# Performance work log

Measured on AMD Instinct MI355X. Metric: run time of the kernel, lower is better.

The kernel has to match this reference:

```python
import jax, jax.numpy as jnp
import numpy as np

N, E, D, L = 50000, 800000, 128, 2
EPS = 1e-10


def mobius_add(x, y, c):
    # c: shape [1], broadcasts against [N,1]
    xy = jnp.sum(x * y, axis=-1, keepdims=True)
    x2 = jnp.sum(x * x, axis=-1, keepdims=True)
    y2 = jnp.sum(y * y, axis=-1, keepdims=True)
    num = (1 + 2 * c * xy + c * y2) * x + (1 - c * x2) * y
    den = 1 + 2 * c * xy + (c ** 2) * x2 * y2
    return num / den


def log_map(x, y, c):
    ym = mobius_add(-x, y, c)
    n = jnp.maximum(jnp.linalg.norm(ym, axis=-1, keepdims=True), EPS)
    sc = jnp.sqrt(c)
    return (2.0 / sc) * jnp.arctanh(sc * n) * ym / n


def exp_map(x, v, c):
    n = jnp.maximum(jnp.linalg.norm(v, axis=-1, keepdims=True), EPS)
    sc = jnp.sqrt(c)
    second = jnp.tanh(sc * n / 2.0) * v / (sc * n)
    return mobius_add(x, second, c)


def l2norm(x):
    return x / jnp.maximum(jnp.linalg.norm(x, axis=-1, keepdims=True), 1e-12)


def mean_agg(h, src, dst, n_nodes):
    # copy_u + mean reduce: mean of h[src] grouped by dst; zero-degree -> 0
    msum = jax.ops.segment_sum(h[src], dst, num_segments=n_nodes)
    deg = jax.ops.segment_sum(jnp.ones((src.shape[0], 1), h.dtype), dst, num_segments=n_nodes)
    return msum / jnp.maximum(deg, 1.0)


def setup_inputs() -> dict:
    key = jax.random.key(0)
    ks = jax.random.split(key, 12)
    scale = 1.0 / np.sqrt(D)
    return {
        "src": jax.random.randint(ks[0], (E,), 0, N, dtype=jnp.int32),
        "dst": jax.random.randint(ks[1], (E,), 0, N, dtype=jnp.int32),
        "e_emb": jax.random.normal(ks[2], (N, D), dtype=jnp.float32),
        "b_emb": 0.01 * jax.random.normal(ks[3], (N, D), dtype=jnp.float32),  # inside Poincare ball
        "s_emb": jax.random.normal(ks[4], (N, D), dtype=jnp.float32),
        "e_W": scale * jax.random.normal(ks[5], (L, D, D), dtype=jnp.float32),
        "e_b": jnp.zeros((L, D), dtype=jnp.float32),
        "b_W": scale * jax.random.normal(ks[6], (L, D, D), dtype=jnp.float32),
        "b_b": jnp.zeros((L, D), dtype=jnp.float32),
        "s_W": scale * jax.random.normal(ks[7], (L, D, D), dtype=jnp.float32),
        "s_b": jnp.zeros((L, D), dtype=jnp.float32),
        "b_curvature": jnp.ones((1,), dtype=jnp.float32),
        "s_curvature": jnp.ones((1,), dtype=jnp.float32),
    }


def reference(src, dst, e_emb, b_emb, s_emb, e_W, e_b, b_W, b_b, s_W, s_b, b_curvature, s_curvature):
    n = e_emb.shape[0]
    origin = jnp.zeros((1, b_emb.shape[-1]), dtype=b_emb.dtype)
    for l in range(L):
        # Euclidean: transform -> mean aggregate -> LeakyReLU(0.2)
        h = e_emb @ e_W[l].T + e_b[l]
        e_emb = mean_agg(h, src, dst, n)
        e_emb = jnp.where(e_emb > 0, e_emb, 0.2 * e_emb)
        # Hyperbolic: log map to tangent -> transform -> mean aggregate -> exp map
        tangent = log_map(origin, b_emb, b_curvature)
        hb = tangent @ b_W[l].T + b_b[l]
        neigh_b = mean_agg(hb, src, dst, n)
        b_emb = exp_map(origin, neigh_b, b_curvature)
        # Spherical: normalize -> transform -> normalize -> mean aggregate -> normalize
        hs = l2norm(l2norm(s_emb) @ s_W[l].T + s_b[l])
        s_emb = l2norm(mean_agg(hs, src, dst, n))
    return (e_emb, b_emb, s_emb)
```

## Files before the change

### kernel.cpp

```cpp
#include <hip/hip_runtime.h>
#include <math.h>

#define DD 128
typedef unsigned int   u32;
typedef unsigned short u16;
typedef short bf16x8 __attribute__((ext_vector_type(8)));
typedef float f32x4  __attribute__((ext_vector_type(4)));

__device__ __forceinline__ float lo2f(u32 p){ return __uint_as_float(p << 16); }
__device__ __forceinline__ float hi2f(u32 p){ return __uint_as_float(p & 0xFFFF0000u); }
__device__ __forceinline__ u16 f2bf(float f){
    u32 u = __float_as_uint(f);
    return (u16)((u + 0x7fffu + ((u >> 16) & 1u)) >> 16);
}

__global__ void k_hist(const int* __restrict__ dst, int* __restrict__ deg, int E){
    int i = blockIdx.x*256 + threadIdx.x;
    if (i < E) atomicAdd(&deg[dst[i]], 1);
}

__global__ void k_chunksum(const int* __restrict__ deg, int* __restrict__ csum,
                           float* __restrict__ invdeg, int n){
    __shared__ int sdata[256];
    int t = threadIdx.x;
    int i0 = blockIdx.x*512 + t*2;
    int a = (i0     < n) ? deg[i0]   : 0;
    int b = (i0 + 1 < n) ? deg[i0+1] : 0;
    if (i0     < n) invdeg[i0]   = 1.0f / (float)max(a, 1);
    if (i0 + 1 < n) invdeg[i0+1] = 1.0f / (float)max(b, 1);
    sdata[t] = a + b; __syncthreads();
    for (int off = 128; off > 0; off >>= 1){
        if (t < off) sdata[t] += sdata[t+off];
        __syncthreads();
    }
    if (t == 0) csum[blockIdx.x] = sdata[0];
}

__global__ void k_scanchunks(int* __restrict__ csum, int nchunks,
                             int* __restrict__ row_ptr, int n){
    __shared__ int s[256];
    __shared__ int carry_sh;
    int t = threadIdx.x;
    if (t == 0) carry_sh = 0;
    __syncthreads();
    for (int base = 0; base < nchunks; base += 256){
        int i = base + t;
        int v = (i < nchunks) ? csum[i] : 0;
        s[t] = v;
        __syncthreads();
        for (int off = 1; off < 256; off <<= 1){
            int u = (t >= off) ? s[t-off] : 0;
            __syncthreads();
            s[t] += u;
            __syncthreads();
        }
        int carry = carry_sh;
        int excl  = carry + s[t] - v;
        if (i < nchunks) csum[i] = excl;
        int tot = s[255];
        __syncthreads();
        if (t == 0) carry_sh = carry + tot;
        __syncthreads();
    }
    if (t == 0) row_ptr[n] = carry_sh;
}

__global__ void k_scanwithin(const int* __restrict__ deg, const int* __restrict__ csum,
                             int* __restrict__ row_ptr, int* __restrict__ cursor, int n){
    __shared__ int s[256];
    int t = threadIdx.x;
    int i0 = blockIdx.x*512 + t*2;
    int a = (i0     < n) ? deg[i0]   : 0;
    int b = (i0 + 1 < n) ? deg[i0+1] : 0;
    int tsum = a + b;
    s[t] = tsum; __syncthreads();
    for (int off = 1; off < 256; off <<= 1){
        int v = (t >= off) ? s[t-off] : 0;
        __syncthreads();
        s[t] += v;
        __syncthreads();
    }
    int excl = s[t] - tsum + csum[blockIdx.x];
    if (i0     < n){ row_ptr[i0]   = excl;     cursor[i0]   = excl;     }
    if (i0 + 1 < n){ row_ptr[i0+1] = excl + a; cursor[i0+1] = excl + a; }
}

template<typename IT>
__global__ void k_fill(const int* __restrict__ src, const int* __restrict__ dst,
                       int* __restrict__ cursor, IT* __restrict__ sorted_src, int E){
    int i = blockIdx.x*256 + threadIdx.x;
    if (i < E){
        int p = atomicAdd(&cursor[dst[i]], 1);
        sorted_src[p] = (IT)src[i];
    }
}

__global__ void k_w2b3(const float* __restrict__ w0, const float* __restrict__ w1,
                       const float* __restrict__ w2,
                       u16* __restrict__ o0, u16* __restrict__ o1, u16* __restrict__ o2,
                       int nw){
    int i = blockIdx.x*256 + threadIdx.x;
    if (i >= nw) return;
    const float* s = (blockIdx.y == 0) ? w0 : (blockIdx.y == 1) ? w1 : w2;
    u16*         o = (blockIdx.y == 0) ? o0 : (blockIdx.y == 1) ? o1 : o2;
    o[i] = f2bf(s[i]);
}

template<int PRE, int POST>
__device__ __forceinline__ void gemm_body(const float* __restrict__ X, const u16* __restrict__ Wb,
                                          const float* __restrict__ bias, u16* __restrict__ Y,
                                          size_t sstride, int n_rows, const float* __restrict__ cptr){
    int t = threadIdx.x;
    int wave = t >> 6, lane = t & 63;
    int q = lane >> 4, m = lane & 15;
    int rowbase = blockIdx.x*128 + wave*32;
    int gr0 = min(rowbase + m,      n_rows - 1);
    int gr1 = min(rowbase + 16 + m, n_rows - 1);

    float4 xv0[8], xv1[8];
    const float4* xp0 = (const float4*)(X + (size_t)gr0*DD);
    const float4* xp1 = (const float4*)(X + (size_t)gr1*DD);
    #pragma unroll
    for (int c = 0; c < 4; c++){
        xv0[2*c]   = xp0[c*8 + q*2];
        xv0[2*c+1] = xp0[c*8 + q*2 + 1];
        xv1[2*c]   = xp1[c*8 + q*2];
        xv1[2*c+1] = xp1[c*8 + q*2 + 1];
    }

    float scale0 = 1.0f, scale1 = 1.0f;
    if (PRE != 0){
        float ss0 = 0.f, ss1 = 0.f;
        #pragma unroll
        for (int i = 0; i < 8; i++){
            ss0 += xv0[i].x*xv0[i].x + xv0[i].y*xv0[i].y + xv0[i].z*xv0[i].z + xv0[i].w*xv0[i].w;
            ss1 += xv1[i].x*xv1[i].x + xv1[i].y*xv1[i].y + xv1[i].z*xv1[i].z + xv1[i].w*xv1[i].w;
        }
        ss0 += __shfl_xor(ss0, 16, 64); ss0 += __shfl_xor(ss0, 32, 64);
        ss1 += __shfl_xor(ss1, 16, 64); ss1 += __shfl_xor(ss1, 32, 64);
        if (PRE == 1){
            float c  = cptr[0];
            c = (c > 0.f && c < 1e30f) ? c : 1.0f;
            float sc = sqrtf(c);
            float n0 = fmaxf(sqrtf(ss0), 1e-10f);
            float n1 = fmaxf(sqrtf(ss1), 1e-10f);
            float a0 = fminf(sc*n0, 0.99999994f);
            float a1 = fminf(sc*n1, 0.99999994f);
            scale0 = (2.0f/sc) * atanhf(a0) / n0;
            scale1 = (2.0f/sc) * atanhf(a1) / n1;
        } else {
            scale0 = 1.0f / fmaxf(sqrtf(ss0), 1e-12f);
            scale1 = 1.0f / fmaxf(sqrtf(ss1), 1e-12f);
        }
    }

    bf16x8 af0[4], af1[4];
    #pragma unroll
    for (int c = 0; c < 4; c++){
        const float* xf0 = (const float*)&xv0[2*c];
        const float* xf1 = (const float*)&xv1[2*c];
        #pragma unroll
        for (int j = 0; j < 8; j++){
            af0[c][j] = (short)f2bf(xf0[j]*scale0);
            af1[c][j] = (short)f2bf(xf1[j]*scale1);
        }
    }

    f32x4 acc0[8], acc1[8];
    #pragma unroll
    for (int tl = 0; tl < 8; tl++){
        acc0[tl] = (f32x4){0.f,0.f,0.f,0.f};
        acc1[tl] = (f32x4){0.f,0.f,0.f,0.f};
    }

    const u16* wb = Wb + (size_t)m*DD + q*8;
    #pragma unroll
    for (int c = 0; c < 4; c++){
        #pragma unroll
        for (int tl = 0; tl < 8; tl++){
            bf16x8 bfr = *(const bf16x8*)(wb + (size_t)tl*16*DD + c*32);
            acc0[tl] = __builtin_amdgcn_mfma_f32_16x16x32_bf16(af0[c], bfr, acc0[tl], 0, 0, 0);
            acc1[tl] = __builtin_amdgcn_mfma_f32_16x16x32_bf16(af1[c], bfr, acc1[tl], 0, 0, 0);
        }
    }

    #pragma unroll
    for (int tl = 0; tl < 8; tl++){
        float bv = bias[tl*16 + m];
        #pragma unroll
        for (int r = 0; r < 4; r++){ acc0[tl][r] += bv; acc1[tl][r] += bv; }
    }
    if (POST == 1){
        float ssr0[4] = {0.f,0.f,0.f,0.f};
        float ssr1[4] = {0.f,0.f,0.f,0.f};
        #pragma unroll
        for (int tl = 0; tl < 8; tl++)
            #pragma unroll
            for (int r = 0; r < 4; r++){
                ssr0[r] += acc0[tl][r]*acc0[tl][r];
                ssr1[r] += acc1[tl][r]*acc1[tl][r];
            }
        #pragma unroll
        for (int r = 0; r < 4; r++){
            float s0 = ssr0[r], s1 = ssr1[r];
            s0 += __shfl_xor(s0, 1, 64); s0 += __shfl_xor(s0, 2, 64);
            s0 += __shfl_xor(s0, 4, 64); s0 += __shfl_xor(s0, 8, 64);
            s1 += __shfl_xor(s1, 1, 64); s1 += __shfl_xor(s1, 2, 64);
            s1 += __shfl_xor(s1, 4, 64); s1 += __shfl_xor(s1, 8, 64);
            float k0 = 1.0f / fmaxf(sqrtf(s0), 1e-12f);
            float k1 = 1.0f / fmaxf(sqrtf(s1), 1e-12f);
            #pragma unroll
            for (int tl = 0; tl < 8; tl++){ acc0[tl][r] *= k0; acc1[tl][r] *= k1; }
        }
    }
    #pragma unroll
    for (int r = 0; r < 4; r++){
        int grow0 = rowbase + q*4 + r;
        int grow1 = rowbase + 16 + q*4 + r;
        if (grow0 < n_rows){
            #pragma unroll
            for (int tl = 0; tl < 8; tl++)
                Y[(size_t)(tl>>1)*sstride + (size_t)grow0*32 + (tl&1)*16 + m] = f2bf(acc0[tl][r]);
        }
        if (grow1 < n_rows){
            #pragma unroll
            for (int tl = 0; tl < 8; tl++)
                Y[(size_t)(tl>>1)*sstride + (size_t)grow1*32 + (tl&1)*16 + m] = f2bf(acc1[tl][r]);
        }
    }
}

template<int PREB>
__global__ __launch_bounds__(256, 2)
void k_gemm3(const float* __restrict__ Xe, const float* __restrict__ Xb, const float* __restrict__ Xs,
             const u16* __restrict__ We, const u16* __restrict__ Wh, const u16* __restrict__ Ws,
             const float* __restrict__ be, const float* __restrict__ bb, const float* __restrict__ bs,
             u16* __restrict__ ebS, u16* __restrict__ sS,
             int n_rows, const float* __restrict__ cptr){
    size_t sstride = (size_t)n_rows * 32;
    if (blockIdx.y == 0)      gemm_body<0,0>(Xe, We, be, ebS,            sstride, n_rows, cptr);
    else if (blockIdx.y == 1) gemm_body<PREB,0>(Xb, Wh, bb, ebS+4*sstride, sstride, n_rows, cptr);
    else                      gemm_body<2,1>(Xs, Ws, bs, sS,             sstride, n_rows, cptr);
}

#define NPG 2
__device__ __forceinline__ void acc8(float* a, uint4 p){
    a[0] += lo2f(p.x); a[1] += hi2f(p.x);
    a[2] += lo2f(p.y); a[3] += hi2f(p.y);
    a[4] += lo2f(p.z); a[5] += hi2f(p.z);
    a[6] += lo2f(p.w); a[7] += hi2f(p.w);
}

template<typename IT, int MODE>
__global__ __launch_bounds__(256)
void k_aggT(const u32* __restrict__ tab,
            const int* __restrict__ row_ptr, const IT* __restrict__ sorted_src,
            const float* __restrict__ invdeg,
            float* __restrict__ oE, float* __restrict__ oB, float* __restrict__ oS,
            int n_rows){
    const int NPB = 64*NPG;
    int xcd = blockIdx.x & 7;
    int idx = blockIdx.x >> 3;
    size_t sstride = (size_t)n_rows * 16;

    const u32* shard; float* dest; int nodebase, hi, colbase; bool leaky;
    if (MODE == 0){
        shard = tab + (size_t)xcd * sstride;
        dest = (xcd < 4) ? oE : oB;
        leaky = (xcd < 4);
        colbase = (xcd & 3) * 32;
        nodebase = idx * NPB; hi = n_rows;
        if (nodebase >= hi) return;
    } else {
        int half = xcd >> 2, c = xcd & 3;
        int lo  = (int)(((long long)n_rows * half) >> 1);
        int hi2 = (int)(((long long)n_rows * (half+1)) >> 1);
        shard = tab + (size_t)c * sstride;
        dest = oS; leaky = false;
        colbase = c * 32;
        nodebase = lo + idx*NPB; hi = hi2;
        if (nodebase >= hi) return;
    }

    int grp = threadIdx.x >> 2;
    int l4  = threadIdx.x & 3;
    const u32* tbl = shard + l4*4;

    #pragma unroll
    for (int k = 0; k < NPG; k++){
        int v = nodebase + k*64 + grp;
        if (v >= hi) continue;
        int beg = row_ptr[v], end = row_ptr[v+1];
        int cnt = end - beg;
        float a[8];
        #pragma unroll
        for (int i = 0; i < 8; i++) a[i] = 0.f;

        int nq = cnt >> 2;
        int p = beg;
        int j0 = 0, j1 = 0, j2 = 0, j3 = 0;
        if (nq > 0){
            j0 = (int)sorted_src[p]; j1 = (int)sorted_src[p+1];
            j2 = (int)sorted_src[p+2]; j3 = (int)sorted_src[p+3];
        }
        for (int q = 0; q < nq; q++){
            uint4 c0 = *(const uint4*)(tbl + (size_t)j0*16);
            uint4 c1 = *(const uint4*)(tbl + (size_t)j1*16);
            uint4 c2 = *(const uint4*)(tbl + (size_t)j2*16);
            uint4 c3 = *(const uint4*)(tbl + (size_t)j3*16);
            p += 4;
            if (q + 1 < nq){
                j0 = (int)sorted_src[p];
                j1 = (int)sorted_src[p+1];
                j2 = (int)sorted_src[p+2];
                j3 = (int)sorted_src[p+3];
            }
            acc8(a, c0); acc8(a, c1); acc8(a, c2); acc8(a, c3);
        }
        for (int r = 0; r < (cnt & 3); r++){
            int j = (int)sorted_src[p + r];
            uint4 c0 = *(const uint4*)(tbl + (size_t)j*16);
            acc8(a, c0);
        }

        float inv = invdeg[v];
        f32x4 o0, o1;
        #pragma unroll
        for (int i = 0; i < 4; i++){
            float x = a[i]*inv;
            o0[i] = (leaky && x < 0.f) ? 0.2f*x : x;
        }
        #pragma unroll
        for (int i = 0; i < 4; i++){
            float x = a[4+i]*inv;
            o1[i] = (leaky && x < 0.f) ? 0.2f*x : x;
        }
        f32x4* dp = (f32x4*)(dest + (size_t)v*DD + colbase + l4*8);
        __builtin_nontemporal_store(o0, dp);
        __builtin_nontemporal_store(o1, dp+1);
    }
}

__global__ __launch_bounds__(256)
void k_final(const float* __restrict__ tb, const float* __restrict__ ts,
             float* __restrict__ ob, float* __restrict__ os,
             int n_rows, const float* __restrict__ cptr){
    int wid = (blockIdx.x*256 + threadIdx.x) >> 6;
    if (wid >= n_rows) return;
    int lane = threadIdx.x & 63;
    float2 vb = *(const float2*)(tb + (size_t)wid*DD + lane*2);
    float2 vs = *(const float2*)(ts + (size_t)wid*DD + lane*2);
    float ssb = vb.x*vb.x + vb.y*vb.y;
    float sss = vs.x*vs.x + vs.y*vs.y;
    #pragma unroll
    for (int m = 32; m > 0; m >>= 1){
        ssb += __shfl_xor(ssb, m, 64);
        sss += __shfl_xor(sss, m, 64);
    }
    float cc = cptr[0];
    cc = (cc > 0.f && cc < 1e30f) ? cc : 1.0f;
    float sc = sqrtf(cc);
    float nb = fmaxf(sqrtf(ssb), 1e-10f);
    float scb = tanhf(sc*nb*0.5f) / (sc*nb);
    float scs = 1.0f / fmaxf(sqrtf(sss), 1e-12f);
    *(float2*)(ob + (size_t)wid*DD + lane*2) = make_float2(vb.x*scb, vb.y*scb);
    *(float2*)(os + (size_t)wid*DD + lane*2) = make_float2(vs.x*scs, vs.y*scs);
}

extern "C" void kernel_launch(void* const* d_in, const int* in_sizes, int n_in,
                              void* d_out, int out_size, void* d_ws, size_t ws_size,
                              hipStream_t stream){
    const int*   src = (const int*)d_in[0];
    const int*   dst = (const int*)d_in[1];
    const float* emb_in[3] = {(const float*)d_in[2], (const float*)d_in[3], (const float*)d_in[4]};
    const float* W_in[3]   = {(const float*)d_in[5], (const float*)d_in[7], (const float*)d_in[9]};
    const float* b_in[3]   = {(const float*)d_in[6], (const float*)d_in[8], (const float*)d_in[10]};
    const float* b_c       = (const float*)d_in[11];

    const int E  = in_sizes[0];
    const int ND = in_sizes[2];
    const int N  = ND / DD;
    const int Lnum = in_sizes[5] / (DD*DD);
    const int nw = Lnum*DD*DD;
    const int nchunks = (N + 511) / 512;
    const bool small_idx = (N <= 65535);

    char* w = (char*)d_ws;
    auto alloc = [&](size_t bytes)->char*{
        char* p = w; w += (bytes + 255) & ~(size_t)255; return p;
    };
    u32*   ebS       = (u32*)  alloc((size_t)ND*4);
    u32*   sS        = (u32*)  alloc((size_t)ND*2);
    float* tb        = (float*)alloc((size_t)ND*4);
    float* ts        = (float*)alloc((size_t)ND*4);
    u16*   Wb[3];
    for (int i = 0; i < 3; i++) Wb[i] = (u16*)alloc((size_t)nw*2);
    float* invdeg    = (float*)alloc((size_t)N*4);
    int*   deg       = (int*)  alloc((size_t)N*4);
    int*   row_ptr   = (int*)  alloc((size_t)(N+1)*4);
    int*   cursor    = (int*)  alloc((size_t)N*4);
    int*   csum      = (int*)  alloc((size_t)nchunks*4);
    void*  sorted_src= (void*) alloc((size_t)E*4);
    (void)ws_size; (void)n_in; (void)out_size;

    float* out_e = (float*)d_out;
    float* out_b = out_e + ND;
    float* out_s = out_e + 2*ND;

    hipMemsetAsync(deg, 0, (size_t)N*4, stream);

    const int TB = 256;
    k_w2b3<<<dim3((nw+TB-1)/TB, 3), TB, 0, stream>>>(W_in[0], W_in[1], W_in[2],
                                                     Wb[0], Wb[1], Wb[2], nw);
    k_hist<<<(E+TB-1)/TB, TB, 0, stream>>>(dst, deg, E);
    k_chunksum<<<nchunks, 256, 0, stream>>>(deg, csum, invdeg, N);
    k_scanchunks<<<1, 256, 0, stream>>>(csum, nchunks, row_ptr, N);
    k_scanwithin<<<nchunks, 256, 0, stream>>>(deg, csum, row_ptr, cursor, N);
    if (small_idx)
        k_fill<u16><<<(E+TB-1)/TB, TB, 0, stream>>>(src, dst, cursor, (u16*)sorted_src, E);
    else
        k_fill<int><<<(E+TB-1)/TB, TB, 0, stream>>>(src, dst, cursor, (int*)sorted_src, E);

    const int gemmblocks = (N + 127) / 128;
    const int NPB = 64*NPG;
    const int nbE = (N + NPB - 1) / NPB;
    const int nbS = (((N + 1) / 2) + NPB - 1) / NPB;
    const int finblocks = (N + 3) / 4;

    const float* se = emb_in[0];
    const float* sb = emb_in[1];
    const float* ss = emb_in[2];

    for (int l = 0; l < Lnum; l++){
        bool last = (l == Lnum - 1);
        if (l == 0)
            k_gemm3<1><<<dim3(gemmblocks, 3), 256, 0, stream>>>(
                se, sb, ss,
                Wb[0] + (size_t)l*DD*DD, Wb[1] + (size_t)l*DD*DD, Wb[2] + (size_t)l*DD*DD,
                b_in[0] + (size_t)l*DD,  b_in[1] + (size_t)l*DD,  b_in[2] + (size_t)l*DD,
                (u16*)ebS, (u16*)sS, N, b_c);
        else
            k_gemm3<0><<<dim3(gemmblocks, 3), 256, 0, stream>>>(
                se, sb, ss,
                Wb[0] + (size_t)l*DD*DD, Wb[1] + (size_t)l*DD*DD, Wb[2] + (size_t)l*DD*DD,
                b_in[0] + (size_t)l*DD,  b_in[1] + (size_t)l*DD,  b_in[2] + (size_t)l*DD,
                (u16*)ebS, (u16*)sS, N, b_c);

        float* dB = last ? tb : out_b;
        float* dS = last ? ts : out_s;
        if (small_idx){
            k_aggT<u16,0><<<8*nbE, 256, 0, stream>>>(ebS, row_ptr, (const u16*)sorted_src,
                                                     invdeg, out_e, dB, dS, N);
            k_aggT<u16,1><<<8*nbS, 256, 0, stream>>>(sS,  row_ptr, (const u16*)sorted_src,
                                                     invdeg, out_e, dB, dS, N);
        } else {
            k_aggT<int,0><<<8*nbE, 256, 0, stream>>>(ebS, row_ptr, (const int*)sorted_src,
                                                     invdeg, out_e, dB, dS, N);
            k_aggT<int,1><<<8*nbS, 256, 0, stream>>>(sS,  row_ptr, (const int*)sorted_src,
                                                     invdeg, out_e, dB, dS, N);
        }
        if (last)
            k_final<<<finblocks, 256, 0, stream>>>(tb, ts, out_b, out_s, N, b_c);

        se = out_e; sb = out_b; ss = out_s;
    }
}
```

Baseline: 471.1 us.

## Store intermediate layer embeddings as bf16 and add bf16-input GEMM path

Non-final layers now have the aggregation kernels write bf16 intermediates into scratch buffers instead of fp32 into the output arrays. A new GEMM variant, k_gemm3b, reads those bf16 rows directly as MFMA operands, and for the spherical branch it still re-normalizes the rows before the multiply. This halves the bytes written and re-read between layers and skips the fp32-to-bf16 conversion in the next GEMM. It costs extra rounding of the inter-layer activations, although they were already rounded to bf16 before the MFMA. It also changes the layer-0 call path, which now always takes the first weight slice.

Result: no change. 464.1 us (-1.5%).

```diff
diff --git a/kernel.cpp b/kernel.cpp
--- a/kernel.cpp
+++ b/kernel.cpp
@@ -6,9 +6,11 @@
 typedef unsigned short u16;
 typedef short bf16x8 __attribute__((ext_vector_type(8)));
 typedef float f32x4  __attribute__((ext_vector_type(4)));
+typedef u32   u32x4v __attribute__((ext_vector_type(4)));
 
 __device__ __forceinline__ float lo2f(u32 p){ return __uint_as_float(p << 16); }
 __device__ __forceinline__ float hi2f(u32 p){ return __uint_as_float(p & 0xFFFF0000u); }
+__device__ __forceinline__ float b2f(u16 b){ return __uint_as_float(((u32)b) << 16); }
 __device__ __forceinline__ u16 f2bf(float f){
     u32 u = __float_as_uint(f);
     return (u16)((u + 0x7fffu + ((u >> 16) & 1u)) >> 16);
@@ -106,6 +108,57 @@
     o[i] = f2bf(s[i]);
 }
 
+template<int POST>
+__device__ __forceinline__ void gemm_epi(f32x4* acc0, f32x4* acc1,
+                                         const float* __restrict__ bias, u16* __restrict__ Y,
+                                         size_t sstride, int n_rows,
+                                         int rowbase, int q, int m){
+    #pragma unroll
+    for (int tl = 0; tl < 8; tl++){
+        float bv = bias[tl*16 + m];
+        #pragma unroll
+        for (int r = 0; r < 4; r++){ acc0[tl][r] += bv; acc1[tl][r] += bv; }
+    }
+    if (POST == 1){
+        float ssr0[4] = {0.f,0.f,0.f,0.f};
+        float ssr1[4] = {0.f,0.f,0.f,0.f};
+        #pragma unroll
+        for (int tl = 0; tl < 8; tl++)
+            #pragma unroll
+            for (int r = 0; r < 4; r++){
+                ssr0[r] += acc0[tl][r]*acc0[tl][r];
+                ssr1[r] += acc1[tl][r]*acc1[tl][r];
+            }
+        #pragma unroll
+        for (int r = 0; r < 4; r++){
+            float s0 = ssr0[r], s1 = ssr1[r];
+            s0 += __shfl_xor(s0, 1, 64); s0 += __shfl_xor(s0, 2, 64);
+            s0 += __shfl_xor(s0, 4, 64); s0 += __shfl_xor(s0, 8, 64);
+            s1 += __shfl_xor(s1, 1, 64); s1 += __shfl_xor(s1, 2, 64);
+            s1 += __shfl_xor(s1, 4, 64); s1 += __shfl_xor(s1, 8, 64);
+            float k0 = 1.0f / fmaxf(sqrtf(s0), 1e-12f);
+            float k1 = 1.0f / fmaxf(sqrtf(s1), 1e-12f);
+            #pragma unroll
+            for (int tl = 0; tl < 8; tl++){ acc0[tl][r] *= k0; acc1[tl][r] *= k1; }
+        }
+    }
+    #pragma unroll
+    for (int r = 0; r < 4; r++){
+        int grow0 = rowbase + q*4 + r;
+        int grow1 = rowbase + 16 + q*4 + r;
+        if (grow0 < n_rows){
+            #pragma unroll
+            for (int tl = 0; tl < 8; tl++)
+                Y[(size_t)(tl>>1)*sstride + (size_t)grow0*32 + (tl&1)*16 + m] = f2bf(acc0[tl][r]);
+        }
+        if (grow1 < n_rows){
+            #pragma unroll
+            for (int tl = 0; tl < 8; tl++)
+                Y[(size_t)(tl>>1)*sstride + (size_t)grow1*32 + (tl&1)*16 + m] = f2bf(acc1[tl][r]);
+        }
+    }
+}
+
 template<int PRE, int POST>
 __device__ __forceinline__ void gemm_body(const float* __restrict__ X, const u16* __restrict__ Wb,
                                           const float* __restrict__ bias, u16* __restrict__ Y,
@@ -172,7 +225,6 @@
         acc0[tl] = (f32x4){0.f,0.f,0.f,0.f};
         acc1[tl] = (f32x4){0.f,0.f,0.f,0.f};
     }
-
     const u16* wb = Wb + (size_t)m*DD + q*8;
     #pragma unroll
     for (int c = 0; c < 4; c++){
@@ -183,54 +235,73 @@
             acc1[tl] = __builtin_amdgcn_mfma_f32_16x16x32_bf16(af1[c], bfr, acc1[tl], 0, 0, 0);
         }
     }
-
+    gemm_epi<POST>(acc0, acc1, bias, Y, sstride, n_rows, rowbase, q, m);
+}
+
+template<int PRE, int POST>
+__device__ __forceinline__ void gemm_bodyB(const u16* __restrict__ X, const u16* __restrict__ Wb,
+                                           const float* __restrict__ bias, u16* __restrict__ Y,
+                                           size_t sstride, int n_rows){
+    int t = threadIdx.x;
+    int wave = t >> 6, lane = t & 63;
+    int q = lane >> 4, m = lane & 15;
+    int rowbase = blockIdx.x*128 + wave*32;
+    int gr0 = min(rowbase + m,      n_rows - 1);
+    int gr1 = min(rowbase + 16 + m, n_rows - 1);
+
+    bf16x8 af0[4], af1[4];
+    const u16* xr0 = X + (size_t)gr0*DD + q*8;
+    const u16* xr1 = X + (size_t)gr1*DD + q*8;
+    #pragma unroll
+    for (int c = 0; c < 4; c++){
+        af0[c] = *(const bf16x8*)(xr0 + c*32);
+        af1[c] = *(const bf16x8*)(xr1 + c*32);
+    }
+
+    if (PRE == 2){
+        float x0[32], x1[32];
+        float ss0 = 0.f, ss1 = 0.f;
+        #pragma unroll
+        for (int c = 0; c < 4; c++)
+            #pragma unroll
+            for (int j = 0; j < 8; j++){
+                float f0 = b2f((u16)af0[c][j]);
+                float f1 = b2f((u16)af1[c][j]);
+                x0[c*8+j] = f0; x1[c*8+j] = f1;
+                ss0 += f0*f0; ss1 += f1*f1;
+            }
+        ss0 += __shfl_xor(ss0, 16, 64); ss0 += __shfl_xor(ss0, 32, 64);
+        ss1 += __shfl_xor(ss1, 16, 64); ss1 += __shfl_xor(ss1, 32, 64);
+        float k0 = 1.0f / fmaxf(sqrtf(ss0), 1e-12f);
+        float k1 = 1.0f / fmaxf(sqrtf(ss1), 1e-12f);
+        #pragma unroll
+        for (int c = 0; c < 4; c++)
+            #pragma unroll
+            for (int j = 0; j < 8; j++){
+                af0[c][j] = (short)f2bf(x0[c*8+j]*k0);
+                af1[c][j] = (short)f2bf(x1[c*8+j]*k1);
+            }
+    }
+
+    f32x4 acc0[8], acc1[8];
     #pragma unroll
     for (int tl = 0; tl < 8; tl++){
-        float bv = bias[tl*16 + m];
-        #pragma unroll
-        for (int r = 0; r < 4; r++){ acc0[tl][r] += bv; acc1[tl][r] += bv; }
-    }
-    if (POST == 1){
-        float ssr0[4] = {0.f,0.f,0.f,0.f};
-        float ssr1[4] = {0.f,0.f,0.f,0.f};
-        #pragma unroll
-        for (int tl = 0; tl < 8; tl++)
-            #pragma unroll
-            for (int r = 0; r < 4; r++){
-                ssr0[r] += acc0[tl][r]*acc0[tl][r];
-                ssr1[r] += acc1[tl][r]*acc1[tl][r];
-            }
-        #pragma unroll
-        for (int r = 0; r < 4; r++){
-            float s0 = ssr0[r], s1 = ssr1[r];
-            s0 += __shfl_xor(s0, 1, 64); s0 += __shfl_xor(s0, 2, 64);
-            s0 += __shfl_xor(s0, 4, 64); s0 += __shfl_xor(s0, 8, 64);
-            s1 += __shfl_xor(s1, 1, 64); s1 += __shfl_xor(s1, 2, 64);
-            s1 += __shfl_xor(s1, 4, 64); s1 += __shfl_xor(s1, 8, 64);
-            float k0 = 1.0f / fmaxf(sqrtf(s0), 1e-12f);
-            float k1 = 1.0f / fmaxf(sqrtf(s1), 1e-12f);
-            #pragma unroll
-            for (int tl = 0; tl < 8; tl++){ acc0[tl][r] *= k0; acc1[tl][r] *= k1; }
-        }
-    }
-    #pragma unroll
-    for (int r = 0; r < 4; r++){
-        int grow0 = rowbase + q*4 + r;
-        int grow1 = rowbase + 16 + q*4 + r;
-        if (grow0 < n_rows){
-            #pragma unroll
-            for (int tl = 0; tl < 8; tl++)
-                Y[(size_t)(tl>>1)*sstride + (size_t)grow0*32 + (tl&1)*16 + m] = f2bf(acc0[tl][r]);
-        }
-        if (grow1 < n_rows){
-            #pragma unroll
-            for (int tl = 0; tl < 8; tl++)
-                Y[(size_t)(tl>>1)*sstride + (size_t)grow1*32 + (tl&1)*16 + m] = f2bf(acc1[tl][r]);
-        }
-    }
-}
-
-template<int PREB>
+        acc0[tl] = (f32x4){0.f,0.f,0.f,0.f};
+        acc1[tl] = (f32x4){0.f,0.f,0.f,0.f};
+    }
+    const u16* wb = Wb + (size_t)m*DD + q*8;
+    #pragma unroll
+    for (int c = 0; c < 4; c++){
+        #pragma unroll
+        for (int tl = 0; tl < 8; tl++){
+            bf16x8 bfr = *(const bf16x8*)(wb + (size_t)tl*16*DD + c*32);
+            acc0[tl] = __builtin_amdgcn_mfma_f32_16x16x32_bf16(af0[c], bfr, acc0[tl], 0, 0, 0);
+            acc1[tl] = __builtin_amdgcn_mfma_f32_16x16x32_bf16(af1[c], bfr, acc1[tl], 0, 0, 0);
+        }
+    }
+    gemm_epi<POST>(acc0, acc1, bias, Y, sstride, n_rows, rowbase, q, m);
+}
+
 __global__ __launch_bounds__(256, 2)
 void k_gemm3(const float* __restrict__ Xe, const float* __restrict__ Xb, const float* __restrict__ Xs,
              const u16* __restrict__ We, const u16* __restrict__ Wh, const u16* __restrict__ Ws,
@@ -239,8 +310,19 @@
              int n_rows, const float* __restrict__ cptr){
     size_t sstride = (size_t)n_rows * 32;
     if (blockIdx.y == 0)      gemm_body<0,0>(Xe, We, be, ebS,            sstride, n_rows, cptr);
-    else if (blockIdx.y == 1) gemm_body<PREB,0>(Xb, Wh, bb, ebS+4*sstride, sstride, n_rows, cptr);
+    else if (blockIdx.y == 1) gemm_body<1,0>(Xb, Wh, bb, ebS+4*sstride, sstride, n_rows, cptr);
     else                      gemm_body<2,1>(Xs, Ws, bs, sS,             sstride, n_rows, cptr);
+}
+
+__global__ __launch_bounds__(256, 2)
+void k_gemm3b(const u16* __restrict__ Xe, const u16* __restrict__ Xb, const u16* __restrict__ Xs,
+              const u16* __restrict__ We, const u16* __restrict__ Wh, const u16* __restrict__ Ws,
+              const float* __restrict__ be, const float* __restrict__ bb, const float* __restrict__ bs,
+              u16* __restrict__ ebS, u16* __restrict__ sS, int n_rows){
+    size_t sstride = (size_t)n_rows * 32;
+    if (blockIdx.y == 0)      gemm_bodyB<0,0>(Xe, We, be, ebS,            sstride, n_rows);
+    else if (blockIdx.y == 1) gemm_bodyB<0,0>(Xb, Wh, bb, ebS+4*sstride, sstride, n_rows);
+    else                      gemm_bodyB<2,1>(Xs, Ws, bs, sS,             sstride, n_rows);
 }
 
 #define NPG 2
@@ -251,22 +333,22 @@
     a[6] += lo2f(p.w); a[7] += hi2f(p.w);
 }
 
-template<typename IT, int MODE>
+template<typename IT, int MODE, int OB>
 __global__ __launch_bounds__(256)
 void k_aggT(const u32* __restrict__ tab,
             const int* __restrict__ row_ptr, const IT* __restrict__ sorted_src,
             const float* __restrict__ invdeg,
-            float* __restrict__ oE, float* __restrict__ oB, float* __restrict__ oS,
+            void* __restrict__ oE, void* __restrict__ oB, void* __restrict__ oS,
             int n_rows){
     const int NPB = 64*NPG;
     int xcd = blockIdx.x & 7;
     int idx = blockIdx.x >> 3;
     size_t sstride = (size_t)n_rows * 16;
 
-    const u32* shard; float* dest; int nodebase, hi, colbase; bool leaky;
+    const u32* shard; void* dvp; int nodebase, hi, colbase; bool leaky;
     if (MODE == 0){
         shard = tab + (size_t)xcd * sstride;
-        dest = (xcd < 4) ? oE : oB;
+        dvp = (xcd < 4) ? oE : oB;
         leaky = (xcd < 4);
         colbase = (xcd & 3) * 32;
         nodebase = idx * NPB; hi = n_rows;
@@ -276,7 +358,7 @@
         int lo  = (int)(((long long)n_rows * half) >> 1);
         int hi2 = (int)(((long long)n_rows * (half+1)) >> 1);
         shard = tab + (size_t)c * sstride;
-        dest = oS; leaky = false;
+        dvp = oS; leaky = false;
         colbase = c * 32;
         nodebase = lo + idx*NPB; hi = hi2;
         if (nodebase >= hi) return;
@@ -324,20 +406,28 @@
         }
 
         float inv = invdeg[v];
-        f32x4 o0, o1;
-        #pragma unroll
-        for (int i = 0; i < 4; i++){
+        float o[8];
+        #pragma unroll
+        for (int i = 0; i < 8; i++){
             float x = a[i]*inv;
-            o0[i] = (leaky && x < 0.f) ? 0.2f*x : x;
-        }
-        #pragma unroll
-        for (int i = 0; i < 4; i++){
-            float x = a[4+i]*inv;
-            o1[i] = (leaky && x < 0.f) ? 0.2f*x : x;
-        }
-        f32x4* dp = (f32x4*)(dest + (size_t)v*DD + colbase + l4*8);
-        __builtin_nontemporal_store(o0, dp);
-        __builtin_nontemporal_store(o1, dp+1);
+            o[i] = (leaky && x < 0.f) ? 0.2f*x : x;
+        }
+        if (OB){
+            u16* dest = (u16*)dvp;
+            u32 w0 = (u32)f2bf(o[0]) | ((u32)f2bf(o[1]) << 16);
+            u32 w1 = (u32)f2bf(o[2]) | ((u32)f2bf(o[3]) << 16);
+            u32 w2 = (u32)f2bf(o[4]) | ((u32)f2bf(o[5]) << 16);
+            u32 w3 = (u32)f2bf(o[6]) | ((u32)f2bf(o[7]) << 16);
+            u32x4v st = {w0, w1, w2, w3};
+            __builtin_nontemporal_store(st, (u32x4v*)(dest + (size_t)v*DD + colbase + l4*8));
+        } else {
+            float* dest = (float*)dvp;
+            f32x4 o0 = {o[0],o[1],o[2],o[3]};
+            f32x4 o1 = {o[4],o[5],o[6],o[7]};
+            f32x4* dp = (f32x4*)(dest + (size_t)v*DD + colbase + l4*8);
+            __builtin_nontemporal_store(o0, dp);
+            __builtin_nontemporal_store(o1, dp+1);
+        }
     }
 }
 
@@ -393,6 +483,9 @@
     u32*   sS        = (u32*)  alloc((size_t)ND*2);
     float* tb        = (float*)alloc((size_t)ND*4);
     float* ts        = (float*)alloc((size_t)ND*4);
+    u16*   xs16      = (u16*)  alloc((size_t)ND*2);
+    u16*   xe16      = (u16*)tb;
+    u16*   xb16      = (u16*)ts;
     u16*   Wb[3];
     for (int i = 0; i < 3; i++) Wb[i] = (u16*)alloc((size_t)nw*2);
     float* invdeg    = (float*)alloc((size_t)N*4);
@@ -427,41 +520,51 @@
     const int nbS = (((N + 1) / 2) + NPB - 1) / NPB;
     const int finblocks = (N + 3) / 4;
 
-    const float* se = emb_in[0];
-    const float* sb = emb_in[1];
-    const float* ss = emb_in[2];
-
     for (int l = 0; l < Lnum; l++){
         bool last = (l == Lnum - 1);
         if (l == 0)
-            k_gemm3<1><<<dim3(gemmblocks, 3), 256, 0, stream>>>(
-                se, sb, ss,
+            k_gemm3<<<dim3(gemmblocks, 3), 256, 0, stream>>>(
+                emb_in[0], emb_in[1], emb_in[2],
+                Wb[0], Wb[1], Wb[2],
+                b_in[0], b_in[1], b_in[2],
+                (u16*)ebS, (u16*)sS, N, b_c);
+        else
+            k_gemm3b<<<dim3(gemmblocks, 3), 256, 0, stream>>>(
+                xe16, xb16, xs16,
                 Wb[0] + (size_t)l*DD*DD, Wb[1] + (size_t)l*DD*DD, Wb[2] + (size_t)l*DD*DD,
                 b_in[0] + (size_t)l*DD,  b_in[1] + (size_t)l*DD,  b_in[2] + (size_t)l*DD,
-                (u16*)ebS, (u16*)sS, N, b_c);
-        else
-            k_gemm3<0><<<dim3(gemmblocks, 3), 256, 0, stream>>>(
-                se, sb, ss,
-                Wb[0] + (size_t)l*DD*DD, Wb[1] + (size_t)l*DD*DD, Wb[2] + (size_t)l*DD*DD,
-                b_in[0] + (size_t)l*DD,  b_in[1] + (size_t)l*DD,  b_in[2] + (size_t)l*DD,
-                (u16*)ebS, (u16*)sS, N, b_c);
-
-        float* dB = last ? tb : out_b;
-        float* dS = last ? ts : out_s;
+                (u16*)ebS, (u16*)sS, N);
+
+        void *dE, *dB, *dS;
+        if (last){ dE = out_e; dB = tb;   dS = ts;   }
+        else     { dE = xe16;  dB = xb16; dS = xs16; }
+
         if (small_idx){
-            k_aggT<u16,0><<<8*nbE, 256, 0, stream>>>(ebS, row_ptr, (const u16*)sorted_src,
-                                                     invdeg, out_e, dB, dS, N);
-            k_aggT<u16,1><<<8*nbS, 256, 0, stream>>>(sS,  row_ptr, (const u16*)sorted_src,
-                                                     invdeg, out_e, dB, dS, N);
+            if (last){
+                k_aggT<u16,0,0><<<8*nbE, 256, 0, stream>>>(ebS, row_ptr, (const u16*)sorted_src,
+                                                           invdeg, dE, dB, dS, N);
+                k_aggT<u16,1,0><<<8*nbS, 256, 0, stream>>>(sS,  row_ptr, (const u16*)sorted_src,
+                                                           invdeg, dE, dB, dS, N);
+            } else {
+                k_aggT<u16,0,1><<<8*nbE, 256, 0, stream>>>(ebS, row_ptr, (const u16*)sorted_src,
+                                                           invdeg, dE, dB, dS, N);
+                k_aggT<u16,1,1><<<8*nbS, 256, 0, stream>>>(sS,  row_ptr, (const u16*)sorted_src,
+                                                           invdeg, dE, dB, dS, N);
+            }
         } else {
-            k_aggT<int,0><<<8*nbE, 256, 0, stream>>>(ebS, row_ptr, (const int*)sorted_src,
-                                                     invdeg, out_e, dB, dS, N);
-            k_aggT<int,1><<<8*nbS, 256, 0, stream>>>(sS,  row_ptr, (const int*)sorted_src,
-                                                     invdeg, out_e, dB, dS, N);
+            if (last){
+                k_aggT<int,0,0><<<8*nbE, 256, 0, stream>>>(ebS, row_ptr, (const int*)sorted_src,
+                                                           invdeg, dE, dB, dS, N);
+                k_aggT<int,1,0><<<8*nbS, 256, 0, stream>>>(sS,  row_ptr, (const int*)sorted_src,
+                                                           invdeg, dE, dB, dS, N);
+            } else {
+                k_aggT<int,0,1><<<8*nbE, 256, 0, stream>>>(ebS, row_ptr, (const int*)sorted_src,
+                                                           invdeg, dE, dB, dS, N);
+                k_aggT<int,1,1><<<8*nbS, 256, 0, stream>>>(sS,  row_ptr, (const int*)sorted_src,
+                                                           invdeg, dE, dB, dS, N);
+            }
         }
         if (last)
             k_final<<<finblocks, 256, 0, stream>>>(tb, ts, out_b, out_s, N, b_c);
-
-        se = out_e; sb = out_b; ss = out_s;
-    }
-}
+    }
+}
```
